# Kernel optimization log

Hardware: AMD Instinct MI355X
Metric: run time of the kernel (lower is better)

The kernel has to match this reference:

```python
import jax, jax.numpy as jnp
import numpy as np

D_MODEL = 1024
NUM_HEADS = 16
DILATION = 2
SEG = 2048


def setup_inputs() -> dict:
    key = jax.random.key(0)
    k1, k2, k3, k4, k5 = jax.random.split(key, 5)
    B, S, D = 2, 8192, D_MODEL
    scale = 1.0 / np.sqrt(D)
    x = jax.random.normal(k1, (B, S, D), dtype=jnp.float32)
    wqkv = jax.random.normal(k2, (D, 3 * D), dtype=jnp.float32) * scale
    bqkv = jnp.zeros((3 * D,), dtype=jnp.float32)
    wo = jax.random.normal(k3, (D, D), dtype=jnp.float32) * scale
    bo = jnp.zeros((D,), dtype=jnp.float32)
    return {"x": x, "wqkv": wqkv, "bqkv": bqkv, "wo": wo, "bo": bo}


def reference(x, wqkv, bqkv, wo, bo):
    B, S, D = x.shape
    H = NUM_HEADS
    hd = D // H
    # segment reshape + dilated strided slice: [B, N, L, D]
    xs = x.reshape(B, -1, SEG, D)[:, :, ::DILATION, :]
    Bn, N, L, _ = xs.shape
    # fused QKV projection
    qkv = xs @ wqkv + bqkv                       # [B, N, L, 3D]
    q, k, v = jnp.split(qkv, 3, axis=-1)
    q = q.reshape(B, N, L, H, hd)
    k = k.reshape(B, N, L, H, hd)
    v = v.reshape(B, N, L, H, hd)
    scale = 1.0 / jnp.sqrt(jnp.asarray(hd, dtype=x.dtype))
    scores = jnp.einsum("bnqhd,bnkhd->bnhqk", q, k) * scale
    attn = jax.nn.softmax(scores, axis=-1)
    out = jnp.einsum("bnhqk,bnkhd->bnqhd", attn, v).reshape(B, N, L, D)
    out = out @ wo + bo                          # out projection
    return out.reshape(B, N * L, D)
```

## Files before the change

### kernel.cpp

```cpp
#include <hip/hip_runtime.h>
#include <hip/hip_bf16.h>
#include <stdint.h>

typedef __attribute__((ext_vector_type(8))) short short8;
typedef __attribute__((ext_vector_type(4))) float float4v;
typedef __attribute__((ext_vector_type(4))) unsigned int uint4v;
typedef unsigned short u16;

#if __has_builtin(__builtin_amdgcn_exp2f)
#define EXP2F(x) __builtin_amdgcn_exp2f(x)
#else
#define EXP2F(x) __expf(0.69314718056f * (x))
#endif

__device__ __forceinline__ u16 f2b(float f) {
    union { __hip_bfloat16 b; u16 u; } cv;
    cv.b = __float2bfloat16(f);
    return cv.u;
}

#define GLD16(g, l) __builtin_amdgcn_global_load_lds( \
    (const __attribute__((address_space(1))) void*)(g), \
    (__attribute__((address_space(3))) void*)(l), 16, 0, 0)

__global__ void convert_x(const float* __restrict__ x, u16* __restrict__ xb) {
    int id = blockIdx.x * 256 + threadIdx.x;
    int row = id >> 8;
    int c4 = id & 255;
    const float4* src = reinterpret_cast<const float4*>(x + (size_t)(2 * row) * 1024) + c4;
    float4 v = *src;
    ushort4 o;
    o.x = f2b(v.x); o.y = f2b(v.y); o.z = f2b(v.z); o.w = f2b(v.w);
    *(reinterpret_cast<ushort4*>(xb + (size_t)row * 1024) + c4) = o;
}

__global__ void transpose_convert(const float* __restrict__ in, u16* __restrict__ out,
                                  int K, int N) {
    __shared__ float tile[32][33];
    int n0 = blockIdx.x * 32, k0 = blockIdx.y * 32;
    int tx = threadIdx.x, ty = threadIdx.y;
#pragma unroll
    for (int i = 0; i < 4; i++)
        tile[ty + i * 8][tx] = in[(size_t)(k0 + ty + i * 8) * N + n0 + tx];
    __syncthreads();
#pragma unroll
    for (int i = 0; i < 4; i++)
        out[(size_t)(n0 + ty + i * 8) * K + k0 + tx] = f2b(tile[tx][ty + i * 8]);
}

template <int MODE>
__global__ __launch_bounds__(256) void gemm_bt(
    const u16* __restrict__ A, const u16* __restrict__ BT,
    const float* __restrict__ bias,
    float* __restrict__ Cf, u16* __restrict__ Cqk, u16* __restrict__ Cvt,
    int M, int N, int K) {
    __shared__ u16 As[128 * 64];
    __shared__ u16 Bs[128 * 64];
    const int tid = threadIdx.x;
    const int w = tid >> 6, l = tid & 63;
    const int q = l >> 4, c = l & 15;
    const int m0 = blockIdx.y * 128, n0 = blockIdx.x * 128;
    const int wm = (w >> 1) * 64, wn = (w & 1) * 64;

    const int srow = w * 8 + (l >> 3);
    const int scol = ((l & 7) ^ (srow & 7)) * 8;
    const u16* gA = A + (size_t)(m0 + srow) * K + scol;
    const u16* gB = BT + (size_t)(n0 + srow) * K + scol;
    char* AsB = (char*)&As[0];
    char* BsB = (char*)&Bs[0];
    const int ldsOff = (w * 8) * 128;

    float4v acc[4][4];
#pragma unroll
    for (int i = 0; i < 4; i++)
#pragma unroll
        for (int j = 0; j < 4; j++) acc[i][j] = {0.f, 0.f, 0.f, 0.f};

    const int cs = c & 7;

    for (int k0 = 0; k0 < K; k0 += 64) {
        __syncthreads();
#pragma unroll
        for (int j = 0; j < 4; j++) {
            GLD16(gA + (size_t)(j * 32) * K + k0, AsB + ldsOff + j * 32 * 128);
            GLD16(gB + (size_t)(j * 32) * K + k0, BsB + ldsOff + j * 32 * 128);
        }
        __syncthreads();
#pragma unroll
        for (int kk = 0; kk < 2; kk++) {
            const int phys = ((kk * 4 + q) ^ cs) * 8;
            short8 af[4], bf[4];
#pragma unroll
            for (int mt = 0; mt < 4; mt++)
                af[mt] = *reinterpret_cast<const short8*>(&As[(wm + mt * 16 + c) * 64 + phys]);
#pragma unroll
            for (int nt = 0; nt < 4; nt++)
                bf[nt] = *reinterpret_cast<const short8*>(&Bs[(wn + nt * 16 + c) * 64 + phys]);
#pragma unroll
            for (int mt = 0; mt < 4; mt++)
#pragma unroll
                for (int nt = 0; nt < 4; nt++)
                    acc[mt][nt] = __builtin_amdgcn_mfma_f32_16x16x32_bf16(af[mt], bf[nt], acc[mt][nt], 0, 0, 0);
        }
    }

    const int q4 = q * 4;
    if (MODE == 0) {
#pragma unroll
        for (int nt = 0; nt < 4; nt++) {
            int col = n0 + wn + nt * 16 + c;
            float bv = bias[col];
#pragma unroll
            for (int mt = 0; mt < 4; mt++) {
                int row = m0 + wm + mt * 16 + q4;
#pragma unroll
                for (int r = 0; r < 4; r++)
                    Cf[(size_t)(row + r) * N + col] = acc[mt][nt][r] + bv;
            }
        }
    } else {
        bool isV = (n0 + wn) >= 2048;
        float qscale = ((n0 + wn) < 1024) ? (0.125f * 1.44269504f) : 1.0f;
#pragma unroll
        for (int nt = 0; nt < 4; nt++) {
            int col = n0 + wn + nt * 16 + c;
            float bv = bias[col];
            if (!isV) {
#pragma unroll
                for (int mt = 0; mt < 4; mt++) {
                    int row = m0 + wm + mt * 16 + q4;
#pragma unroll
                    for (int r = 0; r < 4; r++)
                        Cqk[(size_t)(row + r) * 2048 + col] = f2b((acc[mt][nt][r] + bv) * qscale);
                }
            } else {
                int hd_ = col - 2048;
#pragma unroll
                for (int mt = 0; mt < 4; mt++) {
                    int row = m0 + wm + mt * 16 + q4;
                    int bn = row >> 10, key = row & 1023;
                    ushort4 pk;
                    pk.x = f2b(acc[mt][nt][0] + bv);
                    pk.y = f2b(acc[mt][nt][1] + bv);
                    pk.z = f2b(acc[mt][nt][2] + bv);
                    pk.w = f2b(acc[mt][nt][3] + bv);
                    *reinterpret_cast<ushort4*>(
                        &Cvt[((size_t)(bn << 10) + hd_) * 1024 + key]) = pk;
                }
            }
        }
    }
}

__global__ __launch_bounds__(256) void attn(const u16* __restrict__ qk,
                                            const u16* __restrict__ vt,
                                            u16* __restrict__ ob) {
    __shared__ u16 Ks[64 * 72];
    __shared__ u16 Vs[64 * 72];
    __shared__ u16 Ps[128 * 72];
    const int tid = threadIdx.x;
    const int w = tid >> 6, l = tid & 63, q = l >> 4, c = l & 15;
    const int combo = blockIdx.x, qtile = blockIdx.y;
    const int bn = combo >> 4, h = combo & 15;
    const int t0 = bn << 10;
    const int qoff = h << 6;
    const int koff = 1024 + (h << 6);
    const int vrow0 = combo << 6;
    const int qrow_base = t0 + qtile * 128 + w * 32;

    short8 v1;
    {
        u16 one = (c == 0) ? (u16)0x3F80 : (u16)0;
#pragma unroll
        for (int j = 0; j < 8; j++) v1[j] = (short)one;
    }

    short8 aq[2][2];
#pragma unroll
    for (int mt = 0; mt < 2; mt++)
#pragma unroll
        for (int ks = 0; ks < 2; ks++)
            aq[mt][ks] = *reinterpret_cast<const short8*>(
                qk + (size_t)(qrow_base + mt * 16 + c) * 2048 + qoff + ks * 32 + q * 8);

    float4v o_acc[2][4];
    float4v osum[2];
#pragma unroll
    for (int mt = 0; mt < 2; mt++) {
#pragma unroll
        for (int nt = 0; nt < 4; nt++) o_acc[mt][nt] = {0.f, 0.f, 0.f, 0.f};
        osum[mt] = {0.f, 0.f, 0.f, 0.f};
    }

    const int sr = tid >> 3;
    const int sc = (tid & 7) * 8;

    uint4v kreg[2], vreg[2];
#pragma unroll
    for (int i = 0; i < 2; i++) {
        int r = sr + i * 32;
        kreg[i] = *reinterpret_cast<const uint4v*>(
            qk + (size_t)(t0 + r) * 2048 + koff + sc);
        vreg[i] = *reinterpret_cast<const uint4v*>(
            vt + (size_t)(vrow0 + r) * 1024 + sc);
    }
#pragma unroll
    for (int i = 0; i < 2; i++) {
        int r = sr + i * 32;
        *reinterpret_cast<uint4v*>(&Ks[r * 72 + sc]) = kreg[i];
        *reinterpret_cast<uint4v*>(&Vs[r * 72 + sc]) = vreg[i];
    }
    __syncthreads();

    for (int chunk = 0; chunk < 16; chunk++) {
        if (chunk < 15) {
            const int key0n = (chunk + 1) * 64;
#pragma unroll
            for (int i = 0; i < 2; i++) {
                int r = sr + i * 32;
                kreg[i] = *reinterpret_cast<const uint4v*>(
                    qk + (size_t)(t0 + key0n + r) * 2048 + koff + sc);
                vreg[i] = *reinterpret_cast<const uint4v*>(
                    vt + (size_t)(vrow0 + r) * 1024 + key0n + sc);
            }
        }

        float4v s[2][4];
#pragma unroll
        for (int mt = 0; mt < 2; mt++)
#pragma unroll
            for (int nt = 0; nt < 4; nt++) s[mt][nt] = {0.f, 0.f, 0.f, 0.f};
#pragma unroll
        for (int ks = 0; ks < 2; ks++) {
            short8 bk[4];
#pragma unroll
            for (int nt = 0; nt < 4; nt++)
                bk[nt] = *reinterpret_cast<const short8*>(&Ks[(nt * 16 + c) * 72 + ks * 32 + q * 8]);
#pragma unroll
            for (int mt = 0; mt < 2; mt++)
#pragma unroll
                for (int nt = 0; nt < 4; nt++)
                    s[mt][nt] = __builtin_amdgcn_mfma_f32_16x16x32_bf16(aq[mt][ks], bk[nt], s[mt][nt], 0, 0, 0);
        }

#pragma unroll
        for (int mt = 0; mt < 2; mt++)
#pragma unroll
            for (int r = 0; r < 4; r++)
#pragma unroll
                for (int nt = 0; nt < 4; nt++)
                    Ps[(w * 32 + mt * 16 + q * 4 + r) * 72 + nt * 16 + c] =
                        f2b(EXP2F(s[mt][nt][r]));

#pragma unroll
        for (int ks = 0; ks < 2; ks++) {
            short8 pf[2], vf[4];
#pragma unroll
            for (int mt = 0; mt < 2; mt++)
                pf[mt] = *reinterpret_cast<const short8*>(
                    &Ps[(w * 32 + mt * 16 + c) * 72 + ks * 32 + q * 8]);
#pragma unroll
            for (int nt = 0; nt < 4; nt++)
                vf[nt] = *reinterpret_cast<const short8*>(&Vs[(nt * 16 + c) * 72 + ks * 32 + q * 8]);
#pragma unroll
            for (int mt = 0; mt < 2; mt++) {
#pragma unroll
                for (int nt = 0; nt < 4; nt++)
                    o_acc[mt][nt] = __builtin_amdgcn_mfma_f32_16x16x32_bf16(pf[mt], vf[nt], o_acc[mt][nt], 0, 0, 0);
                osum[mt] = __builtin_amdgcn_mfma_f32_16x16x32_bf16(pf[mt], v1, osum[mt], 0, 0, 0);
            }
        }

        if (chunk < 15) {
            __syncthreads();
#pragma unroll
            for (int i = 0; i < 2; i++) {
                int r = sr + i * 32;
                *reinterpret_cast<uint4v*>(&Ks[r * 72 + sc]) = kreg[i];
                *reinterpret_cast<uint4v*>(&Vs[r * 72 + sc]) = vreg[i];
            }
            __syncthreads();
        }
    }

#pragma unroll
    for (int mt = 0; mt < 2; mt++) {
        float inv[4];
#pragma unroll
        for (int r = 0; r < 4; r++) {
            float lv = __shfl(osum[mt][r], tid & 48);
            inv[r] = 1.0f / lv;
        }
#pragma unroll
        for (int nt = 0; nt < 4; nt++)
#pragma unroll
            for (int r = 0; r < 4; r++) {
                int row = qrow_base + mt * 16 + q * 4 + r;
                int col = (h << 6) + nt * 16 + c;
                ob[(size_t)row * 1024 + col] = f2b(o_acc[mt][nt][r] * inv[r]);
            }
    }
}

extern "C" void kernel_launch(void* const* d_in, const int* in_sizes, int n_in,
                              void* d_out, int out_size, void* d_ws, size_t ws_size,
                              hipStream_t stream) {
    const float* x    = (const float*)d_in[0];
    const float* wqkv = (const float*)d_in[1];
    const float* bqkv = (const float*)d_in[2];
    const float* wo   = (const float*)d_in[3];
    const float* bo   = (const float*)d_in[4];
    float* out = (float*)d_out;
    char* ws = (char*)d_ws;

    u16* xb    = (u16*)(ws);
    u16* wqkvT = (u16*)(ws + 16777216);
    u16* woT   = (u16*)(ws + 23068672);
    u16* qkb   = (u16*)(ws + 25165824);
    u16* vtb   = (u16*)(ws + 58720256);
    u16* obuf  = (u16*)(ws + 75497472);

    convert_x<<<8192, 256, 0, stream>>>(x, xb);
    transpose_convert<<<dim3(96, 32), dim3(32, 8), 0, stream>>>(wqkv, wqkvT, 1024, 3072);
    transpose_convert<<<dim3(32, 32), dim3(32, 8), 0, stream>>>(wo, woT, 1024, 1024);
    gemm_bt<1><<<dim3(24, 64), 256, 0, stream>>>(xb, wqkvT, bqkv,
                                                 nullptr, qkb, vtb, 8192, 3072, 1024);
    attn<<<dim3(128, 8), 256, 0, stream>>>(qkb, vtb, obuf);
    gemm_bt<0><<<dim3(8, 64), 256, 0, stream>>>(obuf, woT, bo,
                                                out, nullptr, nullptr, 8192, 1024, 1024);
}
```

Measured before the change: 259.1 us.

## Merge prep kernels into one launch and halve attention query tile per block

Combines the x conversion and both weight transpose-convert kernels into a single launch that dispatches on block index, cutting launch overhead. Attention blocks now handle 64 query rows (16 per wave) instead of 128, doubling the grid to 2048 blocks to improve occupancy and latency hiding. The trade-off is that each K/V chunk is loaded into shared memory twice as often per query, which raises global and LDS traffic.

After: 268.9 us. +3.8%, slower.

```diff
diff --git a/kernel.cpp b/kernel.cpp
--- a/kernel.cpp
+++ b/kernel.cpp
@@ -23,29 +23,43 @@
     (const __attribute__((address_space(1))) void*)(g), \
     (__attribute__((address_space(3))) void*)(l), 16, 0, 0)
 
-__global__ void convert_x(const float* __restrict__ x, u16* __restrict__ xb) {
-    int id = blockIdx.x * 256 + threadIdx.x;
-    int row = id >> 8;
-    int c4 = id & 255;
-    const float4* src = reinterpret_cast<const float4*>(x + (size_t)(2 * row) * 1024) + c4;
-    float4 v = *src;
-    ushort4 o;
-    o.x = f2b(v.x); o.y = f2b(v.y); o.z = f2b(v.z); o.w = f2b(v.w);
-    *(reinterpret_cast<ushort4*>(xb + (size_t)row * 1024) + c4) = o;
-}
-
-__global__ void transpose_convert(const float* __restrict__ in, u16* __restrict__ out,
-                                  int K, int N) {
+__global__ __launch_bounds__(256) void prep(const float* __restrict__ x, u16* __restrict__ xb,
+                                            const float* __restrict__ wqkv, u16* __restrict__ wqkvT,
+                                            const float* __restrict__ wo, u16* __restrict__ woT) {
+    const int bx = blockIdx.x;
+    const int tid = threadIdx.x;
+    if (bx < 8192) {
+        int id = bx * 256 + tid;
+        int row = id >> 8;
+        int c4 = id & 255;
+        const float4* src = reinterpret_cast<const float4*>(x + (size_t)(2 * row) * 1024) + c4;
+        float4 v = *src;
+        ushort4 o;
+        o.x = f2b(v.x); o.y = f2b(v.y); o.z = f2b(v.z); o.w = f2b(v.w);
+        *(reinterpret_cast<ushort4*>(xb + (size_t)row * 1024) + c4) = o;
+        return;
+    }
     __shared__ float tile[32][33];
-    int n0 = blockIdx.x * 32, k0 = blockIdx.y * 32;
-    int tx = threadIdx.x, ty = threadIdx.y;
+    const float* in;
+    u16* out;
+    int n0, k0, N;
+    if (bx < 8192 + 3072) {
+        int bb = bx - 8192;
+        in = wqkv; out = wqkvT; N = 3072;
+        n0 = (bb % 96) * 32; k0 = (bb / 96) * 32;
+    } else {
+        int bb = bx - 11264;
+        in = wo; out = woT; N = 1024;
+        n0 = (bb & 31) * 32; k0 = (bb >> 5) * 32;
+    }
+    int tx = tid & 31, ty = tid >> 5;
 #pragma unroll
     for (int i = 0; i < 4; i++)
         tile[ty + i * 8][tx] = in[(size_t)(k0 + ty + i * 8) * N + n0 + tx];
     __syncthreads();
 #pragma unroll
     for (int i = 0; i < 4; i++)
-        out[(size_t)(n0 + ty + i * 8) * K + k0 + tx] = f2b(tile[tx][ty + i * 8]);
+        out[(size_t)(n0 + ty + i * 8) * 1024 + k0 + tx] = f2b(tile[tx][ty + i * 8]);
 }
 
 template <int MODE>
@@ -157,7 +171,7 @@
                                             u16* __restrict__ ob) {
     __shared__ u16 Ks[64 * 72];
     __shared__ u16 Vs[64 * 72];
-    __shared__ u16 Ps[128 * 72];
+    __shared__ u16 Ps[64 * 72];
     const int tid = threadIdx.x;
     const int w = tid >> 6, l = tid & 63, q = l >> 4, c = l & 15;
     const int combo = blockIdx.x, qtile = blockIdx.y;
@@ -166,7 +180,7 @@
     const int qoff = h << 6;
     const int koff = 1024 + (h << 6);
     const int vrow0 = combo << 6;
-    const int qrow_base = t0 + qtile * 128 + w * 32;
+    const int qrow_base = t0 + qtile * 64 + w * 16;
 
     short8 v1;
     {
@@ -175,22 +189,16 @@
         for (int j = 0; j < 8; j++) v1[j] = (short)one;
     }
 
-    short8 aq[2][2];
-#pragma unroll
-    for (int mt = 0; mt < 2; mt++)
-#pragma unroll
-        for (int ks = 0; ks < 2; ks++)
-            aq[mt][ks] = *reinterpret_cast<const short8*>(
-                qk + (size_t)(qrow_base + mt * 16 + c) * 2048 + qoff + ks * 32 + q * 8);
-
-    float4v o_acc[2][4];
-    float4v osum[2];
-#pragma unroll
-    for (int mt = 0; mt < 2; mt++) {
-#pragma unroll
-        for (int nt = 0; nt < 4; nt++) o_acc[mt][nt] = {0.f, 0.f, 0.f, 0.f};
-        osum[mt] = {0.f, 0.f, 0.f, 0.f};
-    }
+    short8 aq[2];
+#pragma unroll
+    for (int ks = 0; ks < 2; ks++)
+        aq[ks] = *reinterpret_cast<const short8*>(
+            qk + (size_t)(qrow_base + c) * 2048 + qoff + ks * 32 + q * 8);
+
+    float4v o_acc[4];
+    float4v osum = {0.f, 0.f, 0.f, 0.f};
+#pragma unroll
+    for (int nt = 0; nt < 4; nt++) o_acc[nt] = {0.f, 0.f, 0.f, 0.f};
 
     const int sr = tid >> 3;
     const int sc = (tid & 7) * 8;
@@ -225,11 +233,9 @@
             }
         }
 
-        float4v s[2][4];
-#pragma unroll
-        for (int mt = 0; mt < 2; mt++)
-#pragma unroll
-            for (int nt = 0; nt < 4; nt++) s[mt][nt] = {0.f, 0.f, 0.f, 0.f};
+        float4v s[4];
+#pragma unroll
+        for (int nt = 0; nt < 4; nt++) s[nt] = {0.f, 0.f, 0.f, 0.f};
 #pragma unroll
         for (int ks = 0; ks < 2; ks++) {
             short8 bk[4];
@@ -237,38 +243,27 @@
             for (int nt = 0; nt < 4; nt++)
                 bk[nt] = *reinterpret_cast<const short8*>(&Ks[(nt * 16 + c) * 72 + ks * 32 + q * 8]);
 #pragma unroll
-            for (int mt = 0; mt < 2; mt++)
-#pragma unroll
-                for (int nt = 0; nt < 4; nt++)
-                    s[mt][nt] = __builtin_amdgcn_mfma_f32_16x16x32_bf16(aq[mt][ks], bk[nt], s[mt][nt], 0, 0, 0);
-        }
-
-#pragma unroll
-        for (int mt = 0; mt < 2; mt++)
-#pragma unroll
-            for (int r = 0; r < 4; r++)
-#pragma unroll
-                for (int nt = 0; nt < 4; nt++)
-                    Ps[(w * 32 + mt * 16 + q * 4 + r) * 72 + nt * 16 + c] =
-                        f2b(EXP2F(s[mt][nt][r]));
+            for (int nt = 0; nt < 4; nt++)
+                s[nt] = __builtin_amdgcn_mfma_f32_16x16x32_bf16(aq[ks], bk[nt], s[nt], 0, 0, 0);
+        }
+
+#pragma unroll
+        for (int r = 0; r < 4; r++)
+#pragma unroll
+            for (int nt = 0; nt < 4; nt++)
+                Ps[(w * 16 + q * 4 + r) * 72 + nt * 16 + c] = f2b(EXP2F(s[nt][r]));
 
 #pragma unroll
         for (int ks = 0; ks < 2; ks++) {
-            short8 pf[2], vf[4];
-#pragma unroll
-            for (int mt = 0; mt < 2; mt++)
-                pf[mt] = *reinterpret_cast<const short8*>(
-                    &Ps[(w * 32 + mt * 16 + c) * 72 + ks * 32 + q * 8]);
+            short8 pf, vf[4];
+            pf = *reinterpret_cast<const short8*>(&Ps[(w * 16 + c) * 72 + ks * 32 + q * 8]);
 #pragma unroll
             for (int nt = 0; nt < 4; nt++)
                 vf[nt] = *reinterpret_cast<const short8*>(&Vs[(nt * 16 + c) * 72 + ks * 32 + q * 8]);
 #pragma unroll
-            for (int mt = 0; mt < 2; mt++) {
-#pragma unroll
-                for (int nt = 0; nt < 4; nt++)
-                    o_acc[mt][nt] = __builtin_amdgcn_mfma_f32_16x16x32_bf16(pf[mt], vf[nt], o_acc[mt][nt], 0, 0, 0);
-                osum[mt] = __builtin_amdgcn_mfma_f32_16x16x32_bf16(pf[mt], v1, osum[mt], 0, 0, 0);
-            }
+            for (int nt = 0; nt < 4; nt++)
+                o_acc[nt] = __builtin_amdgcn_mfma_f32_16x16x32_bf16(pf, vf[nt], o_acc[nt], 0, 0, 0);
+            osum = __builtin_amdgcn_mfma_f32_16x16x32_bf16(pf, v1, osum, 0, 0, 0);
         }
 
         if (chunk < 15) {
@@ -283,23 +278,20 @@
         }
     }
 
-#pragma unroll
-    for (int mt = 0; mt < 2; mt++) {
-        float inv[4];
+    float inv[4];
+#pragma unroll
+    for (int r = 0; r < 4; r++) {
+        float lv = __shfl(osum[r], tid & 48);
+        inv[r] = 1.0f / lv;
+    }
+#pragma unroll
+    for (int nt = 0; nt < 4; nt++)
 #pragma unroll
         for (int r = 0; r < 4; r++) {
-            float lv = __shfl(osum[mt][r], tid & 48);
-            inv[r] = 1.0f / lv;
-        }
-#pragma unroll
-        for (int nt = 0; nt < 4; nt++)
-#pragma unroll
-            for (int r = 0; r < 4; r++) {
-                int row = qrow_base + mt * 16 + q * 4 + r;
-                int col = (h << 6) + nt * 16 + c;
-                ob[(size_t)row * 1024 + col] = f2b(o_acc[mt][nt][r] * inv[r]);
-            }
-    }
+            int row = qrow_base + q * 4 + r;
+            int col = (h << 6) + nt * 16 + c;
+            ob[(size_t)row * 1024 + col] = f2b(o_acc[nt][r] * inv[r]);
+        }
 }
 
 extern "C" void kernel_launch(void* const* d_in, const int* in_sizes, int n_in,
@@ -320,12 +312,10 @@
     u16* vtb   = (u16*)(ws + 58720256);
     u16* obuf  = (u16*)(ws + 75497472);
 
-    convert_x<<<8192, 256, 0, stream>>>(x, xb);
-    transpose_convert<<<dim3(96, 32), dim3(32, 8), 0, stream>>>(wqkv, wqkvT, 1024, 3072);
-    transpose_convert<<<dim3(32, 32), dim3(32, 8), 0, stream>>>(wo, woT, 1024, 1024);
+    prep<<<12288, 256, 0, stream>>>(x, xb, wqkv, wqkvT, wo, woT);
     gemm_bt<1><<<dim3(24, 64), 256, 0, stream>>>(xb, wqkvT, bqkv,
                                                  nullptr, qkb, vtb, 8192, 3072, 1024);
-    attn<<<dim3(128, 8), 256, 0, stream>>>(qkb, vtb, obuf);
+    attn<<<dim3(128, 16), 256, 0, stream>>>(qkb, vtb, obuf);
     gemm_bt<0><<<dim3(8, 64), 256, 0, stream>>>(obuf, woT, bo,
                                                 out, nullptr, nullptr, 8192, 1024, 1024);
 }
```
